# Optimization experiments

Measured on AMD Instinct MI355X. Metric: run time of the kernel, lower is better.

## Reference

```python
import jax, jax.numpy as jnp
import numpy as np
from jax import lax

HID = 256
CB_N = 512   # codebook_size
CB_D = 64    # codebook_dim
FC = 6       # force_channels
COMMIT_W = 0.25


def _conv(x, w, b, stride):
    # x: [B,C,H,W], w: [O,I,3,3], 'same'-style padding=1
    y = lax.conv_general_dilated(x, w, (stride, stride), ((1, 1), (1, 1)),
                                 dimension_numbers=('NCHW', 'OIHW', 'NCHW'))
    return y + b[None, :, None, None]


def _silu(x):
    return x * jax.nn.sigmoid(x)


def setup_inputs() -> dict:
    key = jax.random.key(0)
    ks = jax.random.split(key, 8)
    s = 0.05
    force_field = jax.random.normal(ks[0], (8, FC, 256, 256), dtype=jnp.float32)
    w1 = jax.random.normal(ks[1], (HID, FC, 3, 3), dtype=jnp.float32) * s
    b1 = jnp.zeros((HID,), dtype=jnp.float32)
    w2 = jax.random.normal(ks[2], (HID, HID, 3, 3), dtype=jnp.float32) * s
    b2 = jnp.zeros((HID,), dtype=jnp.float32)
    w3 = jax.random.normal(ks[3], (CB_D, HID, 3, 3), dtype=jnp.float32) * s
    b3 = jnp.zeros((CB_D,), dtype=jnp.float32)
    codebook = jax.random.uniform(ks[4], (CB_N, CB_D), dtype=jnp.float32,
                                  minval=-1.0 / CB_N, maxval=1.0 / CB_N)
    return {"force_field": force_field, "w1": w1, "b1": b1, "w2": w2,
            "b2": b2, "w3": w3, "b3": b3, "codebook": codebook}


def reference(force_field, w1, b1, w2, b2, w3, b3, codebook):
    # Encoder: conv(pad1) -> SiLU -> conv(stride2) -> SiLU -> conv(stride2)
    h = _silu(_conv(force_field, w1, b1, 1))
    h = _silu(_conv(h, w2, b2, 2))
    z = _conv(h, w3, b3, 2)                      # [B, CB_D, h, w]
    B, C, hh, ww = z.shape
    z_flat = jnp.transpose(z, (0, 2, 3, 1)).reshape(-1, C)  # [N, CB_D]
    # pairwise squared distances: ||z||^2 + ||c||^2 - 2 z.c
    dists = (jnp.sum(z_flat * z_flat, axis=1, keepdims=True)
             + jnp.sum(codebook * codebook, axis=1)
             - 2.0 * (z_flat @ codebook.T))      # [N, CB_N]
    indices = jnp.argmin(dists, axis=1)          # [N] int
    z_q = codebook[indices].reshape(B, hh, ww, C).transpose(0, 3, 1, 2)
    commitment_loss = (jnp.mean((lax.stop_gradient(z_q) - z) ** 2)
                       + COMMIT_W * jnp.mean((z_q - lax.stop_gradient(z)) ** 2))
    tokens = indices.reshape(B, hh, ww)
    return tokens, commitment_loss
```

## Files before the change

kernel.cpp:

```cpp
#include <hip/hip_runtime.h>
#include <math.h>


#define FC    6
#define HID   256
#define CB_N  512
#define CB_D  64

typedef _Float16 f16x8 __attribute__((ext_vector_type(8)));
typedef _Float16 f16x4 __attribute__((ext_vector_type(4)));
typedef float f32x16 __attribute__((ext_vector_type(16)));

#define H1N_IMG    17105920
#define H2N_IMG    4359168

#define FFP_ROW    260
#define FFP_CI     (258 * FFP_ROW)
#define FFP_IMG    (6 * FFP_CI)

__global__ void fill_sentinel_kernel(float* out, int n) {
    int i = blockIdx.x * 256 + threadIdx.x;
    if (i < n) out[i] = -12345.0f;
}

__global__ void h1n_guard_kernel(unsigned int* h1n, int nslots) {
    int i = blockIdx.x * 256 + threadIdx.x;
    if (i >= nslots * 132096) return;
    int slot = i / 132096;
    int r    = i - slot * 132096;
    unsigned int* base = h1n + (size_t)slot * H1N_IMG;
    if (r < 66560) base[r] = 0u;
    else {
        int r2  = r - 66560;
        int j   = r2 & 3;
        int hl  = (r2 >> 2) & 1;
        int cg  = (r2 >> 3) & 31;
        int row = (r2 >> 8) + 1;
        base[(size_t)row * 66560 + 33280 + cg * 1040 + hl * 520 + j] = 0u;
    }
}

__global__ void h2n_guard_kernel(unsigned int* h2n, int nslots) {
    int i = blockIdx.x * 256 + threadIdx.x;
    if (i >= nslots * 66560) return;
    int slot = i / 66560;
    int r    = i - slot * 66560;
    unsigned int* base = h2n + (size_t)slot * H2N_IMG;
    if (r < 33792) base[r] = 0u;
    else {
        int r2  = r - 33792;
        int j   = r2 & 3;
        int hl  = (r2 >> 2) & 1;
        int cg  = (r2 >> 3) & 31;
        int row = (r2 >> 8) + 1;
        base[(size_t)row * 33792 + 16896 + cg * 528 + hl * 264 + j] = 0u;
    }
}

__global__ void wswz1_kernel(const float* __restrict__ w1, _Float16* __restrict__ wsz) {
    int i = blockIdx.x * 256 + threadIdx.x;
    if (i >= 2 * 4 * 4096) return;
    int j   = i & 7;
    int co_ = (i >> 3) & 127;
    int kc  = (i >> 10) & 1;
    int hf  = (i >> 11) & 1;
    int st  = (i >> 12) & 3;
    int ct  = i >> 14;
    int k   = st * 16 + kc * 8 + j;
    int co  = ct * 128 + co_;
    float v = (k < 54) ? w1[(size_t)co * 54 + k] : 0.f;
    _Float16 h = (_Float16)v;
    _Float16 l = (_Float16)(v - (float)h);
    wsz[i] = hf ? l : h;
}

__global__ void wswz2_kernel(const float* __restrict__ w2, _Float16* __restrict__ wsz) {
    int i = blockIdx.x * 256 + threadIdx.x;
    if (i >= 2 * 144 * 4096) return;
    int j   = i & 7;
    int co_ = (i >> 3) & 127;
    int kc  = (i >> 10) & 1;
    int hf  = (i >> 11) & 1;
    int st  = (i >> 12) % 144;
    int ct  = (i >> 12) / 144;
    int r    = st / 48;
    int kq   = st - r * 48;
    int kc16 = kq / 3;
    int s    = kq - kc16 * 3;
    int ci   = kc16 * 16 + kc * 8 + j;
    int rs   = r * 3 + s;
    float v = w2[(size_t)(ct * 128 + co_) * 2304 + ci * 9 + rs];
    _Float16 h = (_Float16)v;
    _Float16 l = (_Float16)(v - (float)h);
    wsz[i] = hf ? l : h;
}

__global__ void wswz3_kernel(const float* __restrict__ w3, _Float16* __restrict__ wsz) {
    int i = blockIdx.x * 256 + threadIdx.x;
    if (i >= 144 * 2048) return;
    int j  = i & 7;
    int co = (i >> 3) & 63;
    int kc = (i >> 9) & 1;
    int hf = (i >> 10) & 1;
    int st = i >> 11;
    int ci = (st & 15) * 16 + kc * 8 + j;
    int rs = st >> 4;
    float v = w3[(size_t)co * 2304 + ci * 9 + rs];
    _Float16 h = (_Float16)v;
    _Float16 l = (_Float16)(v - (float)h);
    wsz[i] = hf ? l : h;
}

__global__ void cnorm_kernel(const float* __restrict__ cb, float* __restrict__ cn) {
    int j = blockIdx.x * 256 + threadIdx.x;
    if (j < CB_N) {
        const float* p = cb + j * CB_D;
        float s0 = 0.f, s1 = 0.f, s2 = 0.f, s3 = 0.f;
        for (int i = 0; i < CB_D; i += 4) {
            s0 = fmaf(p[i],   p[i],   s0);
            s1 = fmaf(p[i+1], p[i+1], s1);
            s2 = fmaf(p[i+2], p[i+2], s2);
            s3 = fmaf(p[i+3], p[i+3], s3);
        }
        cn[j] = (s0 + s1) + (s2 + s3);
    }
}

__device__ __forceinline__ float silu_f(float v) {
    return v / (1.f + expf(-v));
}

__device__ __forceinline__ unsigned int pack_hl(float v) {
    _Float16 h = (_Float16)v;
    _Float16 l = (_Float16)(v - (float)h);
    unsigned short hb = __builtin_bit_cast(unsigned short, h);
    unsigned short lb = __builtin_bit_cast(unsigned short, l);
    return (unsigned int)hb | ((unsigned int)lb << 16);
}

__device__ __forceinline__ f16x8 as_f16x8(uint4 v) {
    return __builtin_bit_cast(f16x8, v);
}

__device__ __forceinline__ unsigned int ldu32_sb(const char* base, unsigned off, int px) {
    return *(const unsigned int*)(base + (unsigned)__builtin_amdgcn_readfirstlane((int)off) + px * 4);
}

__device__ __forceinline__ void sync_lds() {
    asm volatile("s_waitcnt lgkmcnt(0)\n\ts_barrier" ::: "memory");
}

__global__ __launch_bounds__(256) void ffpack_kernel(const float* __restrict__ ff,
                                                     unsigned int* __restrict__ ffp) {
    const int gw   = (blockIdx.x * 256 + threadIdx.x) >> 6;
    const int lane = threadIdx.x & 63;
    const int y  = gw & 255;
    const int ic = gw >> 8;
    const float* rowp = ff + ((size_t)ic * 256 + y) * 256;
    float4 v = *(const float4*)(rowp + 4 * lane);
    unsigned p0 = pack_hl(v.x), p1 = pack_hl(v.y), p2 = pack_hl(v.z), p3 = pack_hl(v.w);
    unsigned p3p = __shfl_up(p3, 1);
    if (lane == 0) p3p = 0u;
    unsigned int* orow = ffp + ((size_t)ic * 258 + y + 1) * FFP_ROW;
    uint4 o; o.x = p3p; o.y = p0; o.z = p1; o.w = p2;
    *(uint4*)(orow + 4 * lane) = o;
    if (lane == 63) { orow[256] = p3; orow[257] = 0u; }
}

__global__ __launch_bounds__(256) void conv1_mfma_kernel(
        const unsigned int* __restrict__ ffp,
        const _Float16* __restrict__ wsz1,
        const float* __restrict__ bias,
        unsigned int* __restrict__ h1n,
        int b0) {
    __shared__ __align__(16) _Float16 ldsA[2][2][128][8];
    __shared__ __align__(16) _Float16 ldsB[2][128][24];
    __shared__ __align__(16) unsigned int T[64];
    __shared__ float biasl[128];

    const int tid = threadIdx.x;
    const int py  = blockIdx.x >> 1;
    const int xt  = blockIdx.x & 1;
    const int ct  = blockIdx.y;
    const int img = blockIdx.z;

    const unsigned int* ffpi = ffp + (size_t)(b0 + img) * FFP_IMG;
    _Float16* h1f = (_Float16*)(h1n + (size_t)img * H1N_IMG);

    if (tid < 64) {
        int k = tid;
        unsigned off;
        if (k < 54) {
            int ci  = k / 9;
            int tap = k - ci * 9;
            int r   = tap / 3;
            int s   = tap - r * 3;
            off = (unsigned)((((size_t)ci * 258 + py + r) * FFP_ROW + xt * 128 + s) * 4);
        } else {
            off = (unsigned)((xt * 128) * 4);
        }
        T[k] = off;
    }
    if (tid < 128) biasl[tid] = bias[ct * 128 + tid];
    __syncthreads();

    const int lane = tid & 63;
    const int w    = tid >> 6;
    const int cow  = (w >> 1) * 64;
    const int pxw  = (w & 1) * 64;
    const int m_   = lane & 31;
    const int kc   = lane >> 5;
    const int px   = tid & 127;
    const int kh   = tid >> 7;

    f32x16 acc[2][2];
    #pragma unroll
    for (int a = 0; a < 2; a++)
        #pragma unroll
        for (int b = 0; b < 2; b++)
            #pragma unroll
            for (int r = 0; r < 16; r++) acc[a][b][r] = 0.f;

    uint4* aldsf = (uint4*)&ldsA[0][0][0][0];
    const char* gbase = (const char*)ffpi;

    uint4 a0, a1;
    unsigned v0, v1, v2, v3, v4, v5, v6, v7;
    {
        const uint4* ag = (const uint4*)(wsz1 + ((size_t)(ct * 4)) * 4096);
        a0 = ag[tid];
        a1 = ag[tid + 256];
        const int k0 = kh * 8;
        uint4 rb0 = *(const uint4*)&T[k0];
        uint4 rb1 = *(const uint4*)&T[k0 + 4];
        v0 = ldu32_sb(gbase, rb0.x, px); v1 = ldu32_sb(gbase, rb0.y, px);
        v2 = ldu32_sb(gbase, rb0.z, px); v3 = ldu32_sb(gbase, rb0.w, px);
        v4 = ldu32_sb(gbase, rb1.x, px); v5 = ldu32_sb(gbase, rb1.y, px);
        v6 = ldu32_sb(gbase, rb1.z, px); v7 = ldu32_sb(gbase, rb1.w, px);
    }

    for (int t = 0; t < 4; t++) {
        sync_lds();

        aldsf[tid]       = a0;
        aldsf[tid + 256] = a1;
        uint4 bh, bl;
        bh.x = (v0 & 0xffffu) | (v1 << 16);
        bh.y = (v2 & 0xffffu) | (v3 << 16);
        bh.z = (v4 & 0xffffu) | (v5 << 16);
        bh.w = (v6 & 0xffffu) | (v7 << 16);
        bl.x = (v0 >> 16) | (v1 & 0xffff0000u);
        bl.y = (v2 >> 16) | (v3 & 0xffff0000u);
        bl.z = (v4 >> 16) | (v5 & 0xffff0000u);
        bl.w = (v6 >> 16) | (v7 & 0xffff0000u);
        *(uint4*)&ldsB[0][px][kh * 8] = bh;
        *(uint4*)&ldsB[1][px][kh * 8] = bl;

        sync_lds();

        if (t < 3) {
            const uint4* ag = (const uint4*)(wsz1 + ((size_t)(ct * 4 + t + 1)) * 4096);
            a0 = ag[tid];
            a1 = ag[tid + 256];
            const int k0 = (t + 1) * 16 + kh * 8;
            uint4 rb0 = *(const uint4*)&T[k0 & 63];
            uint4 rb1 = *(const uint4*)&T[(k0 + 4) & 63];
            v0 = ldu32_sb(gbase, rb0.x, px); v1 = ldu32_sb(gbase, rb0.y, px);
            v2 = ldu32_sb(gbase, rb0.z, px); v3 = ldu32_sb(gbase, rb0.w, px);
            v4 = ldu32_sb(gbase, rb1.x, px); v5 = ldu32_sb(gbase, rb1.y, px);
            v6 = ldu32_sb(gbase, rb1.z, px); v7 = ldu32_sb(gbase, rb1.w, px);
        }

        f16x8 ah0 = *(const f16x8*)&ldsA[0][kc][cow + m_][0];
        f16x8 ah1 = *(const f16x8*)&ldsA[0][kc][cow + 32 + m_][0];
        f16x8 al0 = *(const f16x8*)&ldsA[1][kc][cow + m_][0];
        f16x8 al1 = *(const f16x8*)&ldsA[1][kc][cow + 32 + m_][0];
        f16x8 xh0 = *(const f16x8*)&ldsB[0][pxw + m_][kc * 8];
        f16x8 xh1 = *(const f16x8*)&ldsB[0][pxw + 32 + m_][kc * 8];
        f16x8 xl0 = *(const f16x8*)&ldsB[1][pxw + m_][kc * 8];
        f16x8 xl1 = *(const f16x8*)&ldsB[1][pxw + 32 + m_][kc * 8];

        acc[0][0] = __builtin_amdgcn_mfma_f32_32x32x16_f16(ah0, xh0, acc[0][0], 0, 0, 0);
        acc[0][1] = __builtin_amdgcn_mfma_f32_32x32x16_f16(ah0, xh1, acc[0][1], 0, 0, 0);
        acc[1][0] = __builtin_amdgcn_mfma_f32_32x32x16_f16(ah1, xh0, acc[1][0], 0, 0, 0);
        acc[1][1] = __builtin_amdgcn_mfma_f32_32x32x16_f16(ah1, xh1, acc[1][1], 0, 0, 0);
        acc[0][0] = __builtin_amdgcn_mfma_f32_32x32x16_f16(ah0, xl0, acc[0][0], 0, 0, 0);
        acc[0][1] = __builtin_amdgcn_mfma_f32_32x32x16_f16(ah0, xl1, acc[0][1], 0, 0, 0);
        acc[1][0] = __builtin_amdgcn_mfma_f32_32x32x16_f16(ah1, xl0, acc[1][0], 0, 0, 0);
        acc[1][1] = __builtin_amdgcn_mfma_f32_32x32x16_f16(ah1, xl1, acc[1][1], 0, 0, 0);
        acc[0][0] = __builtin_amdgcn_mfma_f32_32x32x16_f16(al0, xh0, acc[0][0], 0, 0, 0);
        acc[0][1] = __builtin_amdgcn_mfma_f32_32x32x16_f16(al0, xh1, acc[0][1], 0, 0, 0);
        acc[1][0] = __builtin_amdgcn_mfma_f32_32x32x16_f16(al1, xh0, acc[1][0], 0, 0, 0);
        acc[1][1] = __builtin_amdgcn_mfma_f32_32x32x16_f16(al1, xh1, acc[1][1], 0, 0, 0);
    }

    #pragma unroll
    for (int mt = 0; mt < 2; mt++) {
        #pragma unroll
        for (int nt = 0; nt < 2; nt++) {
            const int pxo = xt * 128 + pxw + nt * 32 + m_;
            const int par = pxo & 1;
            const int xs  = par ? ((pxo + 1) >> 1) : (pxo >> 1);
            _Float16* dst = h1f + (size_t)(py + 1) * 133120 + par * 66560 + xs * 8 + kc * 4;
            #pragma unroll
            for (int q = 0; q < 4; q++) {
                const int cb_ = cow + mt * 32 + 8 * q + 4 * kc;
                const int cg  = (ct * 128 + cow + mt * 32 + 8 * q) >> 3;
                f16x4 oh, ol;
                #pragma unroll
                for (int j = 0; j < 4; j++) {
                    float v = silu_f(acc[mt][nt][4*q+j] + biasl[cb_ + j]);
                    _Float16 h = (_Float16)v;
                    oh[j] = h;
                    ol[j] = (_Float16)(v - (float)h);
                }
                *(f16x4*)(dst + (size_t)cg * 2080)        = oh;
                *(f16x4*)(dst + (size_t)cg * 2080 + 1040) = ol;
            }
        }
    }
}

__global__ __launch_bounds__(256, 4) void conv2_mfma_kernel(
        const unsigned int* __restrict__ h1n,
        const _Float16* __restrict__ wsz2,
        const float* __restrict__ bias,
        unsigned int* __restrict__ h2n) {
    const int tid = threadIdx.x;
    const int py  = blockIdx.x >> 1;
    const int xt  = blockIdx.x & 1;
    const int ct  = blockIdx.y;
    const int img = blockIdx.z;

    const int lane = tid & 63;
    const int w    = tid >> 6;
    const int cow  = (w >> 1) * 64;
    const int pxw  = (w & 1) * 32;
    const int m_   = lane & 31;
    const int kc   = lane >> 5;

    const char* bbase = (const char*)(h1n + (size_t)img * H1N_IMG)
                        + (size_t)kc * 4160 + (size_t)(xt * 64 + pxw + m_) * 16;
    const char* abase = (const char*)wsz2 + (size_t)ct * 144 * 8192
                        + (size_t)kc * 2048 + (size_t)(cow + m_) * 16;

    auto offu = [&](int t) -> unsigned {
        int r    = t / 48;
        int kq   = t - r * 48;
        int kc16 = kq / 3;
        int s    = kq - kc16 * 3;
        return (unsigned)((2 * py + r) * 266240 + (s != 1 ? 133120 : 0)
                          + (s == 2 ? 16 : 0) + kc16 * 8320);
    };

    f32x16 acc[2];
    #pragma unroll
    for (int a = 0; a < 2; a++)
        #pragma unroll
        for (int r = 0; r < 16; r++) acc[a][r] = 0.f;

    uint4 rbh[4], rbl[4];
    #pragma unroll
    for (int i = 0; i < 4; i++) {
        unsigned o = offu(i);
        rbh[i] = *(const uint4*)(bbase + o);
        rbl[i] = *(const uint4*)(bbase + o + 2080);
    }
    uint4 pa0 = *(const uint4*)(abase);
    uint4 pa1 = *(const uint4*)(abase + 512);
    uint4 pa2 = *(const uint4*)(abase + 4096);
    uint4 pa3 = *(const uint4*)(abase + 4096 + 512);

    for (int tb = 0; tb < 144; tb += 4) {
        #pragma unroll
        for (int i = 0; i < 4; i++) {
            const int t = tb + i;
            uint4 cbh = rbh[i], cbl = rbl[i];
            if (t + 4 < 144) {
                unsigned o = offu(t + 4);
                rbh[i] = *(const uint4*)(bbase + o);
                rbl[i] = *(const uint4*)(bbase + o + 2080);
            }
            uint4 ca0 = pa0, ca1 = pa1, ca2 = pa2, ca3 = pa3;
            if (t < 143) {
                const char* ap = abase + (size_t)(t + 1) * 8192;
                pa0 = *(const uint4*)(ap);
                pa1 = *(const uint4*)(ap + 512);
                pa2 = *(const uint4*)(ap + 4096);
                pa3 = *(const uint4*)(ap + 4096 + 512);
            }
            f16x8 ah0 = as_f16x8(ca0);
            f16x8 ah1 = as_f16x8(ca1);
            f16x8 al0 = as_f16x8(ca2);
            f16x8 al1 = as_f16x8(ca3);
            f16x8 xh  = as_f16x8(cbh);
            f16x8 xl  = as_f16x8(cbl);

            acc[0] = __builtin_amdgcn_mfma_f32_32x32x16_f16(ah0, xh, acc[0], 0, 0, 0);
            acc[1] = __builtin_amdgcn_mfma_f32_32x32x16_f16(ah1, xh, acc[1], 0, 0, 0);
            acc[0] = __builtin_amdgcn_mfma_f32_32x32x16_f16(ah0, xl, acc[0], 0, 0, 0);
            acc[1] = __builtin_amdgcn_mfma_f32_32x32x16_f16(ah1, xl, acc[1], 0, 0, 0);
            acc[0] = __builtin_amdgcn_mfma_f32_32x32x16_f16(al0, xh, acc[0], 0, 0, 0);
            acc[1] = __builtin_amdgcn_mfma_f32_32x32x16_f16(al1, xh, acc[1], 0, 0, 0);
        }
    }

    const float* bp = bias + ct * 128;
    _Float16* h2f = (_Float16*)(h2n + (size_t)img * H2N_IMG);
    const int pxo = xt * 64 + pxw + m_;
    const int par = pxo & 1;
    const int xs  = par ? ((pxo + 1) >> 1) : (pxo >> 1);
    _Float16* dst = h2f + (size_t)(py + 1) * 67584 + par * 33792 + xs * 8 + kc * 4;
    #pragma unroll
    for (int mt = 0; mt < 2; mt++) {
        #pragma unroll
        for (int q = 0; q < 4; q++) {
            const int cb_ = cow + mt * 32 + 8 * q + 4 * kc;
            const int cg  = (ct * 128 + cow + mt * 32 + 8 * q) >> 3;
            f16x4 oh, ol;
            #pragma unroll
            for (int j = 0; j < 4; j++) {
                float v = silu_f(acc[mt][4*q+j] + bp[cb_ + j]);
                _Float16 h = (_Float16)v;
                oh[j] = h;
                ol[j] = (_Float16)(v - (float)h);
            }
            *(f16x4*)(dst + (size_t)cg * 1056)       = oh;
            *(f16x4*)(dst + (size_t)cg * 1056 + 528) = ol;
        }
    }
}

__global__ __launch_bounds__(64) void conv3_mfma_kernel(
        const unsigned int* __restrict__ h2n,
        const _Float16* __restrict__ wsz3,
        const float* __restrict__ bias,
        float* __restrict__ z) {
    const int bi  = blockIdx.x;
    const int img = blockIdx.y;
    const int py  = bi >> 2;
    const int ct3 = (bi >> 1) & 1;
    const int pxt = bi & 1;

    const int lane = threadIdx.x;
    const int m_   = lane & 31;
    const int kc   = lane >> 5;

    const char* bbase = (const char*)(h2n + (size_t)img * H2N_IMG);
    const char* abase = (const char*)wsz3 + (size_t)kc * 1024 + (size_t)(ct3 * 32 + m_) * 16;
    const unsigned bfix = (unsigned)(kc * 2112 + (pxt * 32 + m_) * 16);

    auto offu = [&](int t) -> unsigned {
        int rs = t >> 4;
        int r  = (rs * 11) >> 5;
        int s  = rs - 3 * r;
        return (unsigned)((2 * py + r) * 135168 + (s != 1 ? 67584 : 0)
                          + (s == 2 ? 16 : 0) + (t & 15) * 4224);
    };

    f32x16 acc;
    #pragma unroll
    for (int r = 0; r < 16; r++) acc[r] = 0.f;

    uint4 rh[8], rl[8];
    #pragma unroll
    for (int i = 0; i < 8; i++) {
        unsigned o = offu(i);
        rh[i] = *(const uint4*)(bbase + o + bfix);
        rl[i] = *(const uint4*)(bbase + o + bfix + 1056);
    }
    uint4 pa0 = *(const uint4*)(abase);
    uint4 pa1 = *(const uint4*)(abase + 2048);

    for (int tb = 0; tb < 144; tb += 8) {
        #pragma unroll
        for (int i = 0; i < 8; i++) {
            const int t = tb + i;
            uint4 cbh = rh[i], cbl = rl[i];
            if (t + 8 < 144) {
                unsigned o = offu(t + 8);
                rh[i] = *(const uint4*)(bbase + o + bfix);
                rl[i] = *(const uint4*)(bbase + o + bfix + 1056);
            }
            uint4 ca0 = pa0, ca1 = pa1;
            if (t < 143) {
                const char* ap = abase + (size_t)(t + 1) * 4096;
                pa0 = *(const uint4*)(ap);
                pa1 = *(const uint4*)(ap + 2048);
            }
            f16x8 ah = as_f16x8(ca0);
            f16x8 al = as_f16x8(ca1);
            f16x8 xh = as_f16x8(cbh);
            f16x8 xl = as_f16x8(cbl);
            acc = __builtin_amdgcn_mfma_f32_32x32x16_f16(ah, xh, acc, 0, 0, 0);
            acc = __builtin_amdgcn_mfma_f32_32x32x16_f16(ah, xl, acc, 0, 0, 0);
            acc = __builtin_amdgcn_mfma_f32_32x32x16_f16(al, xh, acc, 0, 0, 0);
        }
    }

    const int x = pxt * 32 + m_;
    float* zp = z + (((size_t)img * 64 + py) * 64 + x) * 64;
    #pragma unroll
    for (int q = 0; q < 4; q++) {
        const int co = ct3 * 32 + 8 * q + 4 * kc;
        float4 o;
        o.x = acc[4*q+0] + bias[co + 0];
        o.y = acc[4*q+1] + bias[co + 1];
        o.z = acc[4*q+2] + bias[co + 2];
        o.w = acc[4*q+3] + bias[co + 3];
        *(float4*)(zp + co) = o;
    }
}

__global__ __launch_bounds__(128) void vqpart_kernel(const float* __restrict__ z,
                                                     const float* __restrict__ cb,
                                                     const float* __restrict__ cn,
                                                     float* __restrict__ part_d,
                                                     int* __restrict__ part_i) {
    __shared__ __align__(16) float lds_cb[128 * 64];
    __shared__ float lds_cn[128];

    const int tid = threadIdx.x;
    const int q   = blockIdx.y;
    const int n   = blockIdx.x * 128 + tid;

    #pragma unroll
    for (int i = 0; i < 16; i++) {
        const int f4 = tid + 128 * i;
        *(float4*)&lds_cb[f4 * 4] = *(const float4*)(cb + q * 8192 + f4 * 4);
    }
    lds_cn[tid] = cn[q * 128 + tid];
    __syncthreads();

    float zr[64];
    const float* zp = z + (size_t)n * 64;
    #pragma unroll
    for (int i = 0; i < 16; i++)
        *(float4*)&zr[i * 4] = *(const float4*)(zp + i * 4);

    float zn0 = 0.f, zn1 = 0.f, zn2 = 0.f, zn3 = 0.f;
    #pragma unroll
    for (int i = 0; i < 64; i += 4) {
        zn0 = fmaf(zr[i],   zr[i],   zn0);
        zn1 = fmaf(zr[i+1], zr[i+1], zn1);
        zn2 = fmaf(zr[i+2], zr[i+2], zn2);
        zn3 = fmaf(zr[i+3], zr[i+3], zn3);
    }
    const float znorm = (zn0 + zn1) + (zn2 + zn3);

    float dmin = 1e30f;
    int best = 0;
    for (int j = 0; j < 128; j++) {
        const float* cp = &lds_cb[j * 64];
        float d0 = 0.f, d1 = 0.f, d2 = 0.f, d3 = 0.f;
        #pragma unroll
        for (int i = 0; i < 16; i++) {
            const float4 c4 = *(const float4*)&cp[i * 4];
            d0 = fmaf(zr[i*4],   c4.x, d0);
            d1 = fmaf(zr[i*4+1], c4.y, d1);
            d2 = fmaf(zr[i*4+2], c4.z, d2);
            d3 = fmaf(zr[i*4+3], c4.w, d3);
        }
        const float dot = (d0 + d1) + (d2 + d3);
        const float d = (znorm + lds_cn[j]) - 2.f * dot;
        if (d < dmin) { dmin = d; best = q * 128 + j; }
    }

    part_d[(size_t)q * 32768 + n] = dmin;
    part_i[(size_t)q * 32768 + n] = best;
}

__global__ __launch_bounds__(256) void vqred_kernel(const float* __restrict__ z,
                                                    const float* __restrict__ cb,
                                                    const float* __restrict__ part_d,
                                                    const int* __restrict__ part_i,
                                                    float* __restrict__ tokens_out,
                                                    float* __restrict__ loss_accum) {
    __shared__ float red[4];
    const int tid = threadIdx.x;
    const int n   = blockIdx.x * 256 + tid;

    float dmin = part_d[n];
    int   best = part_i[n];
    #pragma unroll
    for (int q = 1; q < 4; q++) {
        float d = part_d[(size_t)q * 32768 + n];
        int   i = part_i[(size_t)q * 32768 + n];
        if (d < dmin) { dmin = d; best = i; }
    }
    tokens_out[n] = (float)best;

    float zr[64];
    const float* zp = z + (size_t)n * 64;
    #pragma unroll
    for (int i = 0; i < 16; i++)
        *(float4*)&zr[i * 4] = *(const float4*)(zp + i * 4);

    const float* cbest = cb + (size_t)best * 64;
    float l0 = 0.f, l1 = 0.f, l2 = 0.f, l3 = 0.f;
    #pragma unroll
    for (int i = 0; i < 64; i += 4) {
        float t0 = cbest[i]     - zr[i];
        float t1 = cbest[i + 1] - zr[i + 1];
        float t2 = cbest[i + 2] - zr[i + 2];
        float t3 = cbest[i + 3] - zr[i + 3];
        l0 = fmaf(t0, t0, l0);
        l1 = fmaf(t1, t1, l1);
        l2 = fmaf(t2, t2, l2);
        l3 = fmaf(t3, t3, l3);
    }
    float l = (l0 + l1) + (l2 + l3);
    #pragma unroll
    for (int off = 32; off > 0; off >>= 1)
        l += __shfl_down(l, off);
    if ((tid & 63) == 0) red[tid >> 6] = l;
    __syncthreads();
    if (tid == 0)
        atomicAdd(loss_accum, (red[0] + red[1]) + (red[2] + red[3]));
}

__global__ void finalize_kernel(const float* __restrict__ loss_accum,
                                float* __restrict__ out_loss) {
    const float m = loss_accum[0] / 2097152.f;
    out_loss[0] = m + 0.25f * m;
}

extern "C" void kernel_launch(void* const* d_in, const int* in_sizes, int n_in,
                              void* d_out, int out_size, void* d_ws, size_t ws_size,
                              hipStream_t stream) {
    const float* ff = (const float*)d_in[0];
    const float* w1 = (const float*)d_in[1];
    const float* b1 = (const float*)d_in[2];
    const float* w2 = (const float*)d_in[3];
    const float* b2 = (const float*)d_in[4];
    const float* w3 = (const float*)d_in[5];
    const float* b3 = (const float*)d_in[6];
    const float* cb = (const float*)d_in[7];
    float* out = (float*)d_out;
    float* ws  = (float*)d_ws;

    const size_t TAIL = 2097152 + 8 * (size_t)FFP_IMG + 589824 + 147456 + 16384
                      + 512 + 131072 + 131072 + 1;
    auto need_u32 = [&](int nimg) -> size_t {
        return (size_t)nimg * (H1N_IMG + H2N_IMG) + TAIL;
    };

    int nimg;
    if      (ws_size >= need_u32(8) * 4) nimg = 8;
    else if (ws_size >= need_u32(4) * 4) nimg = 4;
    else if (ws_size >= need_u32(2) * 4) nimg = 2;
    else {
        fill_sentinel_kernel<<<(out_size + 255) / 256, 256, 0, stream>>>(out, out_size);
        return;
    }

    unsigned int* h1n  = (unsigned int*)ws;
    unsigned int* h2n  = h1n + (size_t)nimg * H1N_IMG;
    float*        zbuf = (float*)(h2n + (size_t)nimg * H2N_IMG);
    unsigned int* ffp  = (unsigned int*)(zbuf + 2097152);
    _Float16* wsz2 = (_Float16*)(ffp + 8 * (size_t)FFP_IMG);
    _Float16* wsz3 = wsz2 + 1179648;
    _Float16* wsz1 = wsz3 + 294912;
    float*    cn   = (float*)(wsz1 + 32768);
    float*    pd   = cn + 512;
    int*      pi   = (int*)(pd + 131072);
    float*    lacc = (float*)(pi + 131072);

    hipMemsetAsync(ffp, 0, 8 * (size_t)FFP_IMG * 4, stream);
    h1n_guard_kernel<<<(nimg * 132096 + 255) / 256, 256, 0, stream>>>(h1n, nimg);
    h2n_guard_kernel<<<(nimg * 66560 + 255) / 256, 256, 0, stream>>>(h2n, nimg);
    wswz1_kernel<<<(2 * 4 * 4096 + 255) / 256, 256, 0, stream>>>(w1, wsz1);
    wswz2_kernel<<<(2 * 144 * 4096 + 255) / 256, 256, 0, stream>>>(w2, wsz2);
    wswz3_kernel<<<(144 * 2048 + 255) / 256, 256, 0, stream>>>(w3, wsz3);
    cnorm_kernel<<<2, 256, 0, stream>>>(cb, cn);
    ffpack_kernel<<<3072, 256, 0, stream>>>(ff, ffp);

    for (int b0 = 0; b0 < 8; b0 += nimg) {
        conv1_mfma_kernel<<<dim3(512, 2, nimg), 256, 0, stream>>>(ffp, wsz1, b1, h1n, b0);
        conv2_mfma_kernel<<<dim3(256, 2, nimg), 256, 0, stream>>>(h1n, wsz2, b2, h2n);
        conv3_mfma_kernel<<<dim3(256, nimg), 64, 0, stream>>>(
            h2n, wsz3, b3, zbuf + (size_t)b0 * 262144);
    }

    hipMemsetAsync(lacc, 0, sizeof(float), stream);
    vqpart_kernel<<<dim3(256, 4), 128, 0, stream>>>(zbuf, cb, cn, pd, pi);
    vqred_kernel<<<128, 256, 0, stream>>>(zbuf, cb, pd, pi, out, lacc);
    finalize_kernel<<<1, 1, 0, stream>>>(lacc, out + 32768);
}
```

Measured before the change: 1.027 ms.

## Stage conv2 activation tiles through a 4-slot LDS ring shared across waves

conv2 now loads each activation tile cooperatively once per block into a 4-slot LDS ring buffer, instead of every wave reading the same activations from global memory. Loads run several steps ahead, and weight prefetch is now two steps deep. The MFMA block is wrapped in s_setprio, and bias is cached in LDS. This cuts redundant global/L2 traffic for the B operand, at the cost of a block-wide barrier on every K step and some LDS usage.

```diff
diff --git a/kernel.cpp b/kernel.cpp
--- a/kernel.cpp
+++ b/kernel.cpp
@@ -326,11 +326,16 @@
         const _Float16* __restrict__ wsz2,
         const float* __restrict__ bias,
         unsigned int* __restrict__ h2n) {
+    __shared__ __align__(16) char ldsB[4 * 4096];
+    __shared__ float biasl[128];
+
     const int tid = threadIdx.x;
     const int py  = blockIdx.x >> 1;
     const int xt  = blockIdx.x & 1;
     const int ct  = blockIdx.y;
     const int img = blockIdx.z;
+
+    if (tid < 128) biasl[tid] = bias[ct * 128 + tid];
 
     const int lane = tid & 63;
     const int w    = tid >> 6;
@@ -339,10 +344,16 @@
     const int m_   = lane & 31;
     const int kc   = lane >> 5;
 
-    const char* bbase = (const char*)(h1n + (size_t)img * H1N_IMG)
-                        + (size_t)kc * 4160 + (size_t)(xt * 64 + pxw + m_) * 16;
+    const char* bbase = (const char*)(h1n + (size_t)img * H1N_IMG);
     const char* abase = (const char*)wsz2 + (size_t)ct * 144 * 8192
                         + (size_t)kc * 2048 + (size_t)(cow + m_) * 16;
+
+    const int spx = tid & 63;
+    const int skc = (tid >> 6) & 1;
+    const int shl = tid >> 7;
+    const unsigned sgfix = (unsigned)(skc * 4160 + spx * 16 + xt * 1024 + shl * 2080);
+    const unsigned swfix = (unsigned)(shl * 2048 + skc * 1024 + spx * 16);
+    const unsigned rfix0 = (unsigned)(kc * 1024 + (pxw + m_) * 16);
 
     auto offu = [&](int t) -> unsigned {
         int r    = t / 48;
@@ -359,53 +370,75 @@
         #pragma unroll
         for (int r = 0; r < 16; r++) acc[a][r] = 0.f;
 
-    uint4 rbh[4], rbl[4];
-    #pragma unroll
-    for (int i = 0; i < 4; i++) {
-        unsigned o = offu(i);
-        rbh[i] = *(const uint4*)(bbase + o);
-        rbl[i] = *(const uint4*)(bbase + o + 2080);
-    }
-    uint4 pa0 = *(const uint4*)(abase);
-    uint4 pa1 = *(const uint4*)(abase + 512);
-    uint4 pa2 = *(const uint4*)(abase + 4096);
-    uint4 pa3 = *(const uint4*)(abase + 4096 + 512);
+    uint4 W0, W1, W2, W3;
+    uint4 Aa0, Aa1, Aa2, Aa3;
+    uint4 Ab0, Ab1, Ab2, Ab3;
+    {
+        uint4 t0v = *(const uint4*)(bbase + offu(0) + sgfix);
+        uint4 t1v = *(const uint4*)(bbase + offu(1) + sgfix);
+        uint4 t2v = *(const uint4*)(bbase + offu(2) + sgfix);
+        W0 = *(const uint4*)(bbase + offu(3) + sgfix);
+        W1 = *(const uint4*)(bbase + offu(4) + sgfix);
+        W2 = *(const uint4*)(bbase + offu(5) + sgfix);
+        W3 = *(const uint4*)(bbase + offu(6) + sgfix);
+        Aa0 = *(const uint4*)(abase);
+        Aa1 = *(const uint4*)(abase + 512);
+        Aa2 = *(const uint4*)(abase + 4096);
+        Aa3 = *(const uint4*)(abase + 4096 + 512);
+        Ab0 = *(const uint4*)(abase + 8192);
+        Ab1 = *(const uint4*)(abase + 8192 + 512);
+        Ab2 = *(const uint4*)(abase + 8192 + 4096);
+        Ab3 = *(const uint4*)(abase + 8192 + 4096 + 512);
+        *(uint4*)(ldsB + 0 * 4096 + swfix) = t0v;
+        *(uint4*)(ldsB + 1 * 4096 + swfix) = t1v;
+        *(uint4*)(ldsB + 2 * 4096 + swfix) = t2v;
+    }
+    sync_lds();
+
+    auto step = [&](int t, int SLOT, uint4& W,
+                    uint4& A0, uint4& A1, uint4& A2, uint4& A3) {
+        if (t < 141) {
+            char* wslot = ldsB + (((SLOT) + 3) & 3) * 4096;
+            *(uint4*)(wslot + swfix) = W;
+        }
+        if (t < 137) {
+            W = *(const uint4*)(bbase + offu(t + 7) + sgfix);
+        }
+        const char* rslot = ldsB + (SLOT) * 4096;
+        f16x8 xh = *(const f16x8*)(rslot + rfix0);
+        f16x8 xl = *(const f16x8*)(rslot + 2048 + rfix0);
+        uint4 ca0 = A0, ca1 = A1, ca2 = A2, ca3 = A3;
+        if (t < 142) {
+            const char* ap = abase + (size_t)(t + 2) * 8192;
+            A0 = *(const uint4*)(ap);
+            A1 = *(const uint4*)(ap + 512);
+            A2 = *(const uint4*)(ap + 4096);
+            A3 = *(const uint4*)(ap + 4096 + 512);
+        }
+        f16x8 ah0 = as_f16x8(ca0);
+        f16x8 ah1 = as_f16x8(ca1);
+        f16x8 al0 = as_f16x8(ca2);
+        f16x8 al1 = as_f16x8(ca3);
+
+        __builtin_amdgcn_s_setprio(1);
+        acc[0] = __builtin_amdgcn_mfma_f32_32x32x16_f16(ah0, xh, acc[0], 0, 0, 0);
+        acc[1] = __builtin_amdgcn_mfma_f32_32x32x16_f16(ah1, xh, acc[1], 0, 0, 0);
+        acc[0] = __builtin_amdgcn_mfma_f32_32x32x16_f16(ah0, xl, acc[0], 0, 0, 0);
+        acc[1] = __builtin_amdgcn_mfma_f32_32x32x16_f16(ah1, xl, acc[1], 0, 0, 0);
+        acc[0] = __builtin_amdgcn_mfma_f32_32x32x16_f16(al0, xh, acc[0], 0, 0, 0);
+        acc[1] = __builtin_amdgcn_mfma_f32_32x32x16_f16(al1, xh, acc[1], 0, 0, 0);
+        __builtin_amdgcn_s_setprio(0);
+
+        sync_lds();
+    };
 
     for (int tb = 0; tb < 144; tb += 4) {
-        #pragma unroll
-        for (int i = 0; i < 4; i++) {
-            const int t = tb + i;
-            uint4 cbh = rbh[i], cbl = rbl[i];
-            if (t + 4 < 144) {
-                unsigned o = offu(t + 4);
-                rbh[i] = *(const uint4*)(bbase + o);
-                rbl[i] = *(const uint4*)(bbase + o + 2080);
-            }
-            uint4 ca0 = pa0, ca1 = pa1, ca2 = pa2, ca3 = pa3;
-            if (t < 143) {
-                const char* ap = abase + (size_t)(t + 1) * 8192;
-                pa0 = *(const uint4*)(ap);
-                pa1 = *(const uint4*)(ap + 512);
-                pa2 = *(const uint4*)(ap + 4096);
-                pa3 = *(const uint4*)(ap + 4096 + 512);
-            }
-            f16x8 ah0 = as_f16x8(ca0);
-            f16x8 ah1 = as_f16x8(ca1);
-            f16x8 al0 = as_f16x8(ca2);
-            f16x8 al1 = as_f16x8(ca3);
-            f16x8 xh  = as_f16x8(cbh);
-            f16x8 xl  = as_f16x8(cbl);
-
-            acc[0] = __builtin_amdgcn_mfma_f32_32x32x16_f16(ah0, xh, acc[0], 0, 0, 0);
-            acc[1] = __builtin_amdgcn_mfma_f32_32x32x16_f16(ah1, xh, acc[1], 0, 0, 0);
-            acc[0] = __builtin_amdgcn_mfma_f32_32x32x16_f16(ah0, xl, acc[0], 0, 0, 0);
-            acc[1] = __builtin_amdgcn_mfma_f32_32x32x16_f16(ah1, xl, acc[1], 0, 0, 0);
-            acc[0] = __builtin_amdgcn_mfma_f32_32x32x16_f16(al0, xh, acc[0], 0, 0, 0);
-            acc[1] = __builtin_amdgcn_mfma_f32_32x32x16_f16(al1, xh, acc[1], 0, 0, 0);
-        }
-    }
-
-    const float* bp = bias + ct * 128;
+        step(tb + 0, 0, W0, Aa0, Aa1, Aa2, Aa3);
+        step(tb + 1, 1, W1, Ab0, Ab1, Ab2, Ab3);
+        step(tb + 2, 2, W2, Aa0, Aa1, Aa2, Aa3);
+        step(tb + 3, 3, W3, Ab0, Ab1, Ab2, Ab3);
+    }
+
     _Float16* h2f = (_Float16*)(h2n + (size_t)img * H2N_IMG);
     const int pxo = xt * 64 + pxw + m_;
     const int par = pxo & 1;
@@ -420,7 +453,7 @@
             f16x4 oh, ol;
             #pragma unroll
             for (int j = 0; j < 4; j++) {
-                float v = silu_f(acc[mt][4*q+j] + bp[cb_ + j]);
+                float v = silu_f(acc[mt][4*q+j] + biasl[cb_ + j]);
                 _Float16 h = (_Float16)v;
                 oh[j] = h;
                 ol[j] = (_Float16)(v - (float)h);
```

Measured after the change: 1.020 ms. No clear change (-0.7%).
